# Kernel optimization log

Hardware: AMD Instinct MI355X
Metric: run time of the kernel (lower is better)

Reference implementation:

```python
import jax, jax.numpy as jnp
import numpy as np

E = 768      # embed_size
H = 12       # num_heads inside each nn.MultiheadAttention
G = 4        # num_groups
D = E // H   # per-head dim = 64


def setup_inputs() -> dict:
    key = jax.random.key(0)
    ks = jax.random.split(key, 20)
    s = 0.02
    B, S = 2, 2048
    inp = {
        "query": jax.random.normal(ks[0], (B, S, E), jnp.float32),
        "key":   jax.random.normal(ks[1], (B, S, E), jnp.float32),
        "value": jax.random.normal(ks[2], (B, S, E), jnp.float32),
        # outer projections (query_group_proj / key_proj / value_proj)
        "Wqg": jax.random.normal(ks[3], (E, E), jnp.float32) * s,
        "bqg": jnp.zeros((E,), jnp.float32),
        "Wk":  jax.random.normal(ks[4], (E, E), jnp.float32) * s,
        "bk":  jnp.zeros((E,), jnp.float32),
        "Wv":  jax.random.normal(ks[5], (E, E), jnp.float32) * s,
        "bv":  jnp.zeros((E,), jnp.float32),
        # per-group MultiheadAttention params (in_proj split into q/k/v, out_proj)
        "Wq_in": jax.random.normal(ks[6], (G, E, E), jnp.float32) * s,
        "bq_in": jnp.zeros((G, E), jnp.float32),
        "Wk_in": jax.random.normal(ks[7], (G, E, E), jnp.float32) * s,
        "bk_in": jnp.zeros((G, E), jnp.float32),
        "Wv_in": jax.random.normal(ks[8], (G, E, E), jnp.float32) * s,
        "bv_in": jnp.zeros((G, E), jnp.float32),
        "Wout":  jax.random.normal(ks[9], (G, E, E), jnp.float32) * s,
        "bout":  jnp.zeros((G, E), jnp.float32),
    }
    return inp


def reference(query, key, value, Wqg, bqg, Wk, bk, Wv, bv,
              Wq_in, bq_in, Wk_in, bk_in, Wv_in, bv_in, Wout, bout):
    B, S, _ = query.shape
    T = S // G  # tokens per group
    scale = 1.0 / np.sqrt(D).astype(np.float32)

    # outer projections (Linear: x @ W.T + b)
    q = query @ Wqg.T + bqg                         # [B,S,E]
    k = key   @ Wk.T  + bk                          # [B,S,E]
    v = value @ Wv.T  + bv                          # [B,S,E]

    # split query tokens into G interleaved groups (view + permute in source)
    qg = q.reshape(B, T, G, E).transpose(0, 2, 1, 3)  # [B,G,T,E]

    # per-group MHA input projections (batched over groups)
    qi = jnp.einsum('bgte,gfe->bgtf', qg, Wq_in) + bq_in[None, :, None, :]
    ki = jnp.einsum('bse,gfe->bgsf', k,  Wk_in) + bk_in[None, :, None, :]
    vi = jnp.einsum('bse,gfe->bgsf', v,  Wv_in) + bv_in[None, :, None, :]

    qh = qi.reshape(B, G, T, H, D)
    kh = ki.reshape(B, G, S, H, D)
    vh = vi.reshape(B, G, S, H, D)

    scores = jnp.einsum('bgthd,bgshd->bghts', qh, kh) * scale  # [B,G,H,T,S]
    attn = jax.nn.softmax(scores, axis=-1)
    ctx = jnp.einsum('bghts,bgshd->bgthd', attn, vh).reshape(B, G, T, E)

    out_g = jnp.einsum('bgte,gfe->bgtf', ctx, Wout) + bout[None, :, None, :]  # [B,G,T,E]

    # reassemble sequence order (inverse of the grouping permutation)
    out = out_g.transpose(0, 2, 1, 3).reshape(B, S, E)
    return out
```

## Files before the change

### kernel.cpp

```cpp
#include <hip/hip_runtime.h>
#include <hip/hip_bf16.h>


typedef __attribute__((ext_vector_type(8))) short short8;
typedef __attribute__((ext_vector_type(4))) float floatx4;

static __device__ __forceinline__ short f2bf(float f) {
    __bf16 b = (__bf16)f;
    return __builtin_bit_cast(short, b);
}
static __device__ __forceinline__ short8 f8_to_bf8(floatx4 f0, floatx4 f1) {
    short8 s;
    s[0]=f2bf(f0[0]); s[1]=f2bf(f0[1]); s[2]=f2bf(f0[2]); s[3]=f2bf(f0[3]);
    s[4]=f2bf(f1[0]); s[5]=f2bf(f1[1]); s[6]=f2bf(f1[2]); s[7]=f2bf(f1[3]);
    return s;
}
static __device__ __forceinline__ void gload_lds16(const short* g, short* l) {
    __builtin_amdgcn_global_load_lds(
        (const __attribute__((address_space(1))) unsigned int*)g,
        (__attribute__((address_space(3))) unsigned int*)l, 16, 0, 0);
}

__global__ __launch_bounds__(256) void cast_w(
    const float* a0, const float* a1, const float* a2, const float* a3,
    const float* a4, const float* a5, const float* a6, short* dst)
{
    const long U = 589824L;
    const float* ptrs[7] = {a0,a1,a2,a3,a4,a5,a6};
    const long starts[8] = {0, U, 2*U, 3*U, 7*U, 11*U, 15*U, 19*U};
    long i = (long)blockIdx.x * 2048 + (long)threadIdx.x * 8;
    int t = 0;
    while (t < 6 && i >= starts[t + 1]) t++;
    const float* s = ptrs[t] + (i - starts[t]);
    floatx4 f0 = *(const floatx4*)s;
    floatx4 f1 = *(const floatx4*)(s + 4);
    *(short8*)(dst + i) = f8_to_bf8(f0, f1);
}

template<int A_IS_F32, int CMODE, int BIAS_ROW>
static __device__ __forceinline__ void gemm_core(
    const void* __restrict__ Av, const short* __restrict__ Wb,
    const float* __restrict__ bp, void* __restrict__ Cv,
    int lda, int ldc, int bm, int bn, short* As, short* Bs)
{
    const int tid = threadIdx.x, lane = tid & 63, w = tid >> 6;
    const int wm = w & 1, wn = w >> 1;
    const int qr = lane >> 4, lc = lane & 15, x7 = lc & 7;
    const int srow = tid >> 3, schunk = tid & 7, sx = srow & 7;

    const short* Wt = Wb + (long)(bn * 128) * 768;

    floatx4 acc[4][4];
#pragma unroll
    for (int mi = 0; mi < 4; mi++)
#pragma unroll
        for (int ni = 0; ni < 4; ni++) acc[mi][ni] = (floatx4){0.f, 0.f, 0.f, 0.f};

    for (int k0 = 0; k0 < 768; k0 += 64) {
        __syncthreads();
#pragma unroll
        for (int p = 0; p < 4; p++) {
            const int row = p * 32 + srow;
            if (A_IS_F32) {
                const float* ap = (const float*)Av + (long)(bm * 128 + row) * lda + k0 + schunk * 8;
                floatx4 f0 = *(const floatx4*)ap;
                floatx4 f1 = *(const floatx4*)(ap + 4);
                *(short8*)&As[row * 64 + ((schunk ^ sx) << 3)] = f8_to_bf8(f0, f1);
            } else {
                gload_lds16((const short*)Av + (long)(bm * 128 + row) * lda + k0 + ((schunk ^ sx) << 3),
                            &As[(p * 32 + w * 8) * 64]);
            }
            gload_lds16(Wt + (long)row * 768 + k0 + ((schunk ^ sx) << 3),
                        &Bs[(p * 32 + w * 8) * 64]);
        }
        __syncthreads();
#pragma unroll
        for (int ks = 0; ks < 64; ks += 32) {
            const int c0 = (ks >> 3) + qr;
            const int slot = ((c0 ^ x7) << 3);
            short8 af[4], bfr[4];
#pragma unroll
            for (int mi = 0; mi < 4; mi++)
                af[mi] = *(const short8*)&As[(wm * 64 + mi * 16 + lc) * 64 + slot];
#pragma unroll
            for (int ni = 0; ni < 4; ni++)
                bfr[ni] = *(const short8*)&Bs[(wn * 64 + ni * 16 + lc) * 64 + slot];
#pragma unroll
            for (int mi = 0; mi < 4; mi++)
#pragma unroll
                for (int ni = 0; ni < 4; ni++)
                    acc[mi][ni] = __builtin_amdgcn_mfma_f32_16x16x32_bf16(
                        af[mi], bfr[ni], acc[mi][ni], 0, 0, 0);
        }
    }

#pragma unroll
    for (int ni = 0; ni < 4; ni++) {
        const int gcol = bn * 128 + wn * 64 + ni * 16 + lc;
        const float bcol = BIAS_ROW ? 0.f : bp[gcol];
#pragma unroll
        for (int mi = 0; mi < 4; mi++) {
#pragma unroll
            for (int r = 0; r < 4; r++) {
                const int grow = bm * 128 + wm * 64 + mi * 16 + qr * 4 + r;
                const float bb = BIAS_ROW ? bp[grow] : bcol;
                const float v = acc[mi][ni][r] + bb;
                if (CMODE == 0)
                    ((short*)Cv)[(long)grow * ldc + gcol] = f2bf(v);
                else
                    ((float*)Cv)[(long)grow * ldc + gcol] = v;
            }
        }
    }
}

__global__ __launch_bounds__(256) void qkv_gemm(
    const float* q, const float* k, const float* v, const short* Wbf,
    const float* bq, const float* bk, const float* bv, short* outp)
{
    __shared__ short As[128 * 64];
    __shared__ short Bs[128 * 64];
    const int xcd = blockIdx.x & 7, slot = blockIdx.x >> 3;
    const int bm = xcd * 4 + slot / 18;
    const int rem = slot % 18, y = rem / 6, bn = rem % 6;
    const float* A    = (y == 0) ? q  : (y == 1) ? k  : v;
    const float* bias = (y == 0) ? bq : (y == 1) ? bk : bv;
    gemm_core<1, 0, 0>(A, Wbf + (long)y * 589824, bias, outp + (long)y * 3145728,
                       768, 768, bm, bn, As, Bs);
}

__global__ __launch_bounds__(256) void mid_gemm(
    const short* kproj, const short* vproj, const short* qproj, const short* Wbf,
    const float* bq_in, const float* bk_in, const float* bv_in,
    short* kiB, short* vtB, short* qiB)
{
    __shared__ short As[128 * 64];
    __shared__ short Bs[128 * 64];
    const int xcd = blockIdx.x & 7, slot = blockIdx.x >> 3;
    const int z = xcd, b = z >> 2, g = z & 3;
    if (slot < 96) {
        gemm_core<0, 0, 0>(kproj + (long)b * 1572864, Wbf + (long)(7 + g) * 589824,
                           bk_in + g * 768, kiB + (long)z * 1572864,
                           768, 768, slot / 6, slot % 6, As, Bs);
    } else if (slot < 192) {
        const int s2 = slot - 96;
        gemm_core<0, 0, 1>(Wbf + (long)(11 + g) * 589824, vproj + (long)b * 1572864,
                           bv_in + g * 768, vtB + (long)z * 1572864,
                           768, 2048, s2 / 16, s2 % 16, As, Bs);
    } else {
        const int s3 = slot - 192;
        gemm_core<0, 0, 0>(qproj + (long)b * 1572864 + g * 768, Wbf + (long)(3 + g) * 589824,
                           bq_in + g * 768, qiB + (long)z * 393216,
                           3072, 768, s3 / 6, s3 % 6, As, Bs);
    }
}

__global__ __launch_bounds__(256) void out_gemm(
    const short* ctxB, const short* Wbf, const float* bout, float* out)
{
    __shared__ short As[128 * 64];
    __shared__ short Bs[128 * 64];
    const int xcd = blockIdx.x & 7, slot = blockIdx.x >> 3;
    const int z = xcd, b = z >> 2, g = z & 3;
    gemm_core<0, 2, 0>(ctxB + (long)z * 393216, Wbf + (long)(15 + g) * 589824,
                       bout + g * 768, out + (long)b * 1572864 + g * 768,
                       768, 3072, slot / 6, slot % 6, As, Bs);
}

__global__ __launch_bounds__(256) void attn_kernel(
    const short* __restrict__ qi, const short* __restrict__ ki,
    const short* __restrict__ vt, short* __restrict__ ctx)
{
    __shared__ short Kt[2][64 * 64];
    __shared__ short Vt[2][64 * 64];
    __shared__ short Ps[4][16 * 64];

    const int tid = threadIdx.x, lane = tid & 63, w = tid >> 6;
    const int qr = lane >> 4, lc = lane & 15, x7 = lc & 7;
    const int headid = blockIdx.x % 96;
    const int tile = blockIdx.x / 96;
    const int h = headid % 12, bg = headid / 12;

    const short* qp = qi + ((long)bg * 512 + tile * 64 + w * 16 + lc) * 768 + h * 64 + qr * 8;
    const short8 aq0 = *(const short8*)qp;
    const short8 aq1 = *(const short8*)(qp + 32);

    const short one = (lc == 0) ? (short)0x3F80 : (short)0;
    const short8 onesv = (short8){one, one, one, one, one, one, one, one};

    floatx4 cacc[4], lacc = (floatx4){0.f, 0.f, 0.f, 0.f};
#pragma unroll
    for (int dc = 0; dc < 4; dc++) cacc[dc] = (floatx4){0.f, 0.f, 0.f, 0.f};

    const int srow = lane >> 3, schk = lane & 7, swz = schk ^ srow;
    const short* kgb = ki + ((long)bg * 2048) * 768 + h * 64;
    const short* vgb = vt + ((long)(bg * 768 + h * 64)) * 2048;

#pragma unroll
    for (int inst = 0; inst < 2; inst++) {
        const int rk = w * 16 + inst * 8 + srow;
        gload_lds16(kgb + (long)rk * 768 + swz * 8, &Kt[0][(w * 16 + inst * 8) * 64]);
        gload_lds16(vgb + (long)rk * 2048 + swz * 8, &Vt[0][(w * 16 + inst * 8) * 64]);
    }

    for (int it = 0; it < 32; it++) {
        const int cur = it & 1;
        __syncthreads();
        if (it < 31) {
            const int nxt = cur ^ 1, s0 = (it + 1) * 64;
#pragma unroll
            for (int inst = 0; inst < 2; inst++) {
                const int rk = w * 16 + inst * 8 + srow;
                gload_lds16(kgb + (long)(s0 + rk) * 768 + swz * 8,
                            &Kt[nxt][(w * 16 + inst * 8) * 64]);
                gload_lds16(vgb + (long)rk * 2048 + s0 + swz * 8,
                            &Vt[nxt][(w * 16 + inst * 8) * 64]);
            }
        }

        const short* Kb = &Kt[cur][0];
        const short* Vb = &Vt[cur][0];

        floatx4 sv[4];
#pragma unroll
        for (int ss = 0; ss < 4; ss++) {
            const short* kr = Kb + (ss * 16 + lc) * 64;
            short8 b0 = *(const short8*)(kr + ((qr ^ x7) << 3));
            short8 b1 = *(const short8*)(kr + (((4 + qr) ^ x7) << 3));
            floatx4 t = (floatx4){0.f, 0.f, 0.f, 0.f};
            t = __builtin_amdgcn_mfma_f32_16x16x32_bf16(aq0, b0, t, 0, 0, 0);
            t = __builtin_amdgcn_mfma_f32_16x16x32_bf16(aq1, b1, t, 0, 0, 0);
            sv[ss] = t;
        }

        short* ps = &Ps[w][0];
#pragma unroll
        for (int ss = 0; ss < 4; ss++) {
            const int cch = ss * 2 + (lc >> 3);
#pragma unroll
            for (int r = 0; r < 4; r++) {
                const int m = qr * 4 + r;
                ps[m * 64 + ((cch ^ (m & 7)) << 3) + x7] =
                    f2bf(__builtin_amdgcn_exp2f(sv[ss][r] * 0.18033688f));
            }
        }
        asm volatile("s_waitcnt lgkmcnt(0)" ::: "memory");
        const short8 ap0 = *(const short8*)&ps[lc * 64 + ((qr ^ x7) << 3)];
        const short8 ap1 = *(const short8*)&ps[lc * 64 + (((4 + qr) ^ x7) << 3)];

        lacc = __builtin_amdgcn_mfma_f32_16x16x32_bf16(ap0, onesv, lacc, 0, 0, 0);
        lacc = __builtin_amdgcn_mfma_f32_16x16x32_bf16(ap1, onesv, lacc, 0, 0, 0);
#pragma unroll
        for (int dc = 0; dc < 4; dc++) {
            const short* vr = Vb + (dc * 16 + lc) * 64;
            short8 bv0 = *(const short8*)(vr + ((qr ^ x7) << 3));
            short8 bv1 = *(const short8*)(vr + (((4 + qr) ^ x7) << 3));
            cacc[dc] = __builtin_amdgcn_mfma_f32_16x16x32_bf16(ap0, bv0, cacc[dc], 0, 0, 0);
            cacc[dc] = __builtin_amdgcn_mfma_f32_16x16x32_bf16(ap1, bv1, cacc[dc], 0, 0, 0);
        }
    }

    float linv[4];
#pragma unroll
    for (int r = 0; r < 4; r++)
        linv[r] = 1.f / __shfl(lacc[r], lane & 48);
    short* cp = ctx + ((long)bg * 512 + tile * 64 + w * 16) * 768 + h * 64;
#pragma unroll
    for (int dc = 0; dc < 4; dc++)
#pragma unroll
        for (int r = 0; r < 4; r++)
            cp[(qr * 4 + r) * 768 + dc * 16 + lc] = f2bf(cacc[dc][r] * linv[r]);
}

extern "C" void kernel_launch(void* const* d_in, const int* in_sizes, int n_in,
                              void* d_out, int out_size, void* d_ws, size_t ws_size,
                              hipStream_t stream) {
    const float* query = (const float*)d_in[0];
    const float* key   = (const float*)d_in[1];
    const float* value = (const float*)d_in[2];
    const float* Wqg = (const float*)d_in[3];  const float* bqg = (const float*)d_in[4];
    const float* Wk  = (const float*)d_in[5];  const float* bk  = (const float*)d_in[6];
    const float* Wv  = (const float*)d_in[7];  const float* bv  = (const float*)d_in[8];
    const float* Wq_in = (const float*)d_in[9];  const float* bq_in = (const float*)d_in[10];
    const float* Wk_in = (const float*)d_in[11]; const float* bk_in = (const float*)d_in[12];
    const float* Wv_in = (const float*)d_in[13]; const float* bv_in = (const float*)d_in[14];
    const float* Wout  = (const float*)d_in[15]; const float* bout  = (const float*)d_in[16];
    float* out = (float*)d_out;

    short* ws     = (short*)d_ws;
    short* Wbf    = ws;
    short* q_proj = ws + 11206656L;
    short* k_proj = ws + 14352384L;
    short* v_proj = ws + 17498112L;
    short* qiB    = ws + 20643840L;
    short* vtB    = ws + 23789568L;
    short* kiB    = ws + 36372480L;
    short* ctxB   = ws + 11206656L;

    dim3 blk(256);

    cast_w<<<dim3(5472), blk, 0, stream>>>(
        Wqg, Wk, Wv, Wq_in, Wk_in, Wv_in, Wout, Wbf);

    qkv_gemm<<<dim3(576), blk, 0, stream>>>(
        query, key, value, Wbf, bqg, bk, bv, q_proj);

    mid_gemm<<<dim3(1728), blk, 0, stream>>>(
        k_proj, v_proj, q_proj, Wbf, bq_in, bk_in, bv_in, kiB, vtB, qiB);

    attn_kernel<<<dim3(768), blk, 0, stream>>>(qiB, kiB, vtB, ctxB);

    out_gemm<<<dim3(192), blk, 0, stream>>>(ctxB, Wbf, bout, out);
}
```

Before: 319.3 us.

## Fold outer projections into per-group input weights to remove a GEMM stage

Precomputes combined weights W2 = W_in·W_outer (per group and per q/k/v) with a small GEMM, and folded biases b2 = W_in·b_outer + b_in. The activations are then projected once through W2 instead of through two chained GEMMs, which removes the qkv_gemm stage and its intermediate buffers. Inputs are cast to bf16 in a prep kernel that also transposes the outer weights. This adds weight-combination work on every call plus a cast pass over the activations, and rounding W2 to bf16 changes the numerics slightly.

```diff
diff --git a/kernel.cpp b/kernel.cpp
--- a/kernel.cpp
+++ b/kernel.cpp
@@ -21,23 +21,66 @@
         (__attribute__((address_space(3))) unsigned int*)l, 16, 0, 0);
 }
 
-__global__ __launch_bounds__(256) void cast_w(
-    const float* a0, const float* a1, const float* a2, const float* a3,
-    const float* a4, const float* a5, const float* a6, short* dst)
-{
+__global__ __launch_bounds__(256) void prep(
+    const float* query, const float* key, const float* value,
+    const float* Wqg, const float* Wk, const float* Wv, const float* Wout,
+    const float* Wq_in, const float* Wk_in, const float* Wv_in,
+    const float* bqg, const float* bk, const float* bv,
+    const float* bq_in, const float* bk_in, const float* bv_in,
+    short* WTo, short* Woutbf, short* qkvbf, float* b2)
+{
+    const int x = blockIdx.x, tid = threadIdx.x;
     const long U = 589824L;
-    const float* ptrs[7] = {a0,a1,a2,a3,a4,a5,a6};
-    const long starts[8] = {0, U, 2*U, 3*U, 7*U, 11*U, 15*U, 19*U};
-    long i = (long)blockIdx.x * 2048 + (long)threadIdx.x * 8;
-    int t = 0;
-    while (t < 6 && i >= starts[t + 1]) t++;
-    const float* s = ptrs[t] + (i - starts[t]);
-    floatx4 f0 = *(const floatx4*)s;
-    floatx4 f1 = *(const floatx4*)(s + 4);
-    *(short8*)(dst + i) = f8_to_bf8(f0, f1);
-}
-
-template<int A_IS_F32, int CMODE, int BIAS_ROW>
+    if (x < 432) {
+        __shared__ float T[64][65];
+        const int mat = x / 144, t = x % 144, tr = t / 12, tc = t % 12;
+        const float* src = (mat == 0) ? Wqg : (mat == 1) ? Wk : Wv;
+        short* dst = WTo + (long)mat * U;
+        const int r = tid >> 2, c0 = (tid & 3) << 4;
+        const float* sp = src + (long)(tr * 64 + r) * 768 + tc * 64 + c0;
+#pragma unroll
+        for (int j = 0; j < 4; j++)
+            *(floatx4*)&T[r][c0 + j * 4] = *(const floatx4*)(sp + j * 4);
+        __syncthreads();
+        short tmp[16];
+#pragma unroll
+        for (int j = 0; j < 16; j++) tmp[j] = f2bf(T[c0 + j][r]);
+        short* dp = dst + (long)(tc * 64 + r) * 768 + tr * 64 + c0;
+        *(short8*)dp = *(short8*)&tmp[0];
+        *(short8*)(dp + 8) = *(short8*)&tmp[8];
+    } else if (x < 1584) {
+        const long i = (long)(x - 432) * 2048 + tid * 8;
+        floatx4 f0 = *(const floatx4*)(Wout + i);
+        floatx4 f1 = *(const floatx4*)(Wout + i + 4);
+        *(short8*)(Woutbf + i) = f8_to_bf8(f0, f1);
+    } else if (x < 6192) {
+        const long i = (long)(x - 1584) * 2048 + tid * 8;
+        const int which = (int)(i / 3145728L);
+        const float* src = (which == 0) ? query : (which == 1) ? key : value;
+        const long off = i - (long)which * 3145728L;
+        floatx4 f0 = *(const floatx4*)(src + off);
+        floatx4 f1 = *(const floatx4*)(src + off + 4);
+        *(short8*)(qkvbf + i) = f8_to_bf8(f0, f1);
+    } else {
+        const int idx = x - 6192, cg = idx >> 2, qtr = idx & 3;
+        const int chain = cg >> 2, g = cg & 3;
+        const float* Wi = ((chain == 0) ? Wq_in : (chain == 1) ? Wk_in : Wv_in) + (long)g * U;
+        const float* bo = (chain == 0) ? bqg : (chain == 1) ? bk : bv;
+        const float* bi = ((chain == 0) ? bq_in : (chain == 1) ? bk_in : bv_in) + g * 768;
+        if (tid < 192) {
+            const int row = qtr * 192 + tid;
+            float acc = 0.f;
+            for (int e = 0; e < 768; e += 4) {
+                floatx4 w = *(const floatx4*)(Wi + (long)row * 768 + e);
+                floatx4 bb = *(const floatx4*)(bo + e);
+                acc += w[0]*bb[0] + w[1]*bb[1] + w[2]*bb[2] + w[3]*bb[3];
+            }
+            b2[cg * 768 + row] = acc + bi[row];
+        }
+    }
+}
+
+template<int A_IS_F32, int CMODE, int BIAS_MODE>
 static __device__ __forceinline__ void gemm_core(
     const void* __restrict__ Av, const short* __restrict__ Wb,
     const float* __restrict__ bp, void* __restrict__ Cv,
@@ -97,13 +140,13 @@
 #pragma unroll
     for (int ni = 0; ni < 4; ni++) {
         const int gcol = bn * 128 + wn * 64 + ni * 16 + lc;
-        const float bcol = BIAS_ROW ? 0.f : bp[gcol];
+        const float bcol = (BIAS_MODE == 0) ? bp[gcol] : 0.f;
 #pragma unroll
         for (int mi = 0; mi < 4; mi++) {
 #pragma unroll
             for (int r = 0; r < 4; r++) {
                 const int grow = bm * 128 + wm * 64 + mi * 16 + qr * 4 + r;
-                const float bb = BIAS_ROW ? bp[grow] : bcol;
+                const float bb = (BIAS_MODE == 1) ? bp[grow] : bcol;
                 const float v = acc[mi][ni][r] + bb;
                 if (CMODE == 0)
                     ((short*)Cv)[(long)grow * ldc + gcol] = f2bf(v);
@@ -114,55 +157,58 @@
     }
 }
 
-__global__ __launch_bounds__(256) void qkv_gemm(
-    const float* q, const float* k, const float* v, const short* Wbf,
-    const float* bq, const float* bk, const float* bv, short* outp)
-{
+__global__ __launch_bounds__(256) void combine_gemm(
+    const float* Wq_in, const float* Wk_in, const float* Wv_in,
+    const short* WTo, short* W2)
+{
+    const int xcd = blockIdx.x & 7, slot = blockIdx.x >> 3;
+    int cg;
+    if (slot < 36) cg = xcd;
+    else { if (xcd >= 4) return; cg = 8 + xcd; }
+    const int tile = slot % 36, chain = cg / 4, g = cg & 3;
     __shared__ short As[128 * 64];
     __shared__ short Bs[128 * 64];
-    const int xcd = blockIdx.x & 7, slot = blockIdx.x >> 3;
-    const int bm = xcd * 4 + slot / 18;
-    const int rem = slot % 18, y = rem / 6, bn = rem % 6;
-    const float* A    = (y == 0) ? q  : (y == 1) ? k  : v;
-    const float* bias = (y == 0) ? bq : (y == 1) ? bk : bv;
-    gemm_core<1, 0, 0>(A, Wbf + (long)y * 589824, bias, outp + (long)y * 3145728,
-                       768, 768, bm, bn, As, Bs);
-}
-
-__global__ __launch_bounds__(256) void mid_gemm(
-    const short* kproj, const short* vproj, const short* qproj, const short* Wbf,
-    const float* bq_in, const float* bk_in, const float* bv_in,
+    const float* A = ((chain == 0) ? Wq_in : (chain == 1) ? Wk_in : Wv_in) + (long)g * 589824;
+    gemm_core<1, 0, 2>(A, WTo + (long)chain * 589824, nullptr,
+                       W2 + (long)cg * 589824, 768, 768, tile / 6, tile % 6, As, Bs);
+}
+
+__global__ __launch_bounds__(256) void proj_gemm(
+    const short* qkvbf, const short* W2, const float* b2,
     short* kiB, short* vtB, short* qiB)
 {
     __shared__ short As[128 * 64];
     __shared__ short Bs[128 * 64];
     const int xcd = blockIdx.x & 7, slot = blockIdx.x >> 3;
     const int z = xcd, b = z >> 2, g = z & 3;
+    const short* q_bf = qkvbf;
+    const short* k_bf = qkvbf + 3145728L;
+    const short* v_bf = qkvbf + 6291456L;
     if (slot < 96) {
-        gemm_core<0, 0, 0>(kproj + (long)b * 1572864, Wbf + (long)(7 + g) * 589824,
-                           bk_in + g * 768, kiB + (long)z * 1572864,
+        gemm_core<0, 0, 0>(k_bf + (long)b * 1572864, W2 + (long)(4 + g) * 589824,
+                           b2 + (4 + g) * 768, kiB + (long)z * 1572864,
                            768, 768, slot / 6, slot % 6, As, Bs);
     } else if (slot < 192) {
         const int s2 = slot - 96;
-        gemm_core<0, 0, 1>(Wbf + (long)(11 + g) * 589824, vproj + (long)b * 1572864,
-                           bv_in + g * 768, vtB + (long)z * 1572864,
+        gemm_core<0, 0, 1>(W2 + (long)(8 + g) * 589824, v_bf + (long)b * 1572864,
+                           b2 + (8 + g) * 768, vtB + (long)z * 1572864,
                            768, 2048, s2 / 16, s2 % 16, As, Bs);
     } else {
         const int s3 = slot - 192;
-        gemm_core<0, 0, 0>(qproj + (long)b * 1572864 + g * 768, Wbf + (long)(3 + g) * 589824,
-                           bq_in + g * 768, qiB + (long)z * 393216,
+        gemm_core<0, 0, 0>(q_bf + (long)b * 1572864 + g * 768, W2 + (long)g * 589824,
+                           b2 + g * 768, qiB + (long)z * 393216,
                            3072, 768, s3 / 6, s3 % 6, As, Bs);
     }
 }
 
 __global__ __launch_bounds__(256) void out_gemm(
-    const short* ctxB, const short* Wbf, const float* bout, float* out)
+    const short* ctxB, const short* Woutbf, const float* bout, float* out)
 {
     __shared__ short As[128 * 64];
     __shared__ short Bs[128 * 64];
     const int xcd = blockIdx.x & 7, slot = blockIdx.x >> 3;
     const int z = xcd, b = z >> 2, g = z & 3;
-    gemm_core<0, 2, 0>(ctxB + (long)z * 393216, Wbf + (long)(15 + g) * 589824,
+    gemm_core<0, 2, 0>(ctxB + (long)z * 393216, Woutbf + (long)g * 589824,
                        bout + g * 768, out + (long)b * 1572864 + g * 768,
                        768, 3072, slot / 6, slot % 6, As, Bs);
 }
@@ -288,27 +334,28 @@
     float* out = (float*)d_out;
 
     short* ws     = (short*)d_ws;
-    short* Wbf    = ws;
-    short* q_proj = ws + 11206656L;
-    short* k_proj = ws + 14352384L;
-    short* v_proj = ws + 17498112L;
+    const long U  = 589824L;
+    short* WTo    = ws;
+    short* Woutbf = ws + 3 * U;
+    short* W2     = ws + 7 * U;
+    short* qkvbf  = ws + 11206656L;
     short* qiB    = ws + 20643840L;
     short* vtB    = ws + 23789568L;
     short* kiB    = ws + 36372480L;
     short* ctxB   = ws + 11206656L;
+    float* b2     = (float*)(ws + 48955392L);
 
     dim3 blk(256);
 
-    cast_w<<<dim3(5472), blk, 0, stream>>>(
-        Wqg, Wk, Wv, Wq_in, Wk_in, Wv_in, Wout, Wbf);
-
-    qkv_gemm<<<dim3(576), blk, 0, stream>>>(
-        query, key, value, Wbf, bqg, bk, bv, q_proj);
-
-    mid_gemm<<<dim3(1728), blk, 0, stream>>>(
-        k_proj, v_proj, q_proj, Wbf, bq_in, bk_in, bv_in, kiB, vtB, qiB);
+    prep<<<dim3(6240), blk, 0, stream>>>(
+        query, key, value, Wqg, Wk, Wv, Wout, Wq_in, Wk_in, Wv_in,
+        bqg, bk, bv, bq_in, bk_in, bv_in, WTo, Woutbf, qkvbf, b2);
+
+    combine_gemm<<<dim3(576), blk, 0, stream>>>(Wq_in, Wk_in, Wv_in, WTo, W2);
+
+    proj_gemm<<<dim3(1728), blk, 0, stream>>>(qkvbf, W2, b2, kiB, vtB, qiB);
 
     attn_kernel<<<dim3(768), blk, 0, stream>>>(qiB, kiB, vtB, ctxB);
 
-    out_gemm<<<dim3(192), blk, 0, stream>>>(ctxB, Wbf, bout, out);
-}
+    out_gemm<<<dim3(192), blk, 0, stream>>>(ctxB, Woutbf, bout, out);
+}
```

After: 348.6 us. +9.2%, slower.
